# Kernel optimization log

Measured on AMD Instinct MI355X. Metric: run time of the kernel, lower is better.

The kernel has to match this reference:

```python
import jax, jax.numpy as jnp
import numpy as np

EPS = 1e-05


def setup_inputs() -> dict:
    key = jax.random.key(0)
    k1, k2 = jax.random.split(key)
    B, H, N, D = 4, 16, 4096, 128
    x = jax.random.normal(k1, (B, H, N, D), dtype=jnp.float32)
    # learned raw (non-skew) parameter; skew-symmetrized in reference
    S_raw = jax.random.normal(k2, (H, D, D), dtype=jnp.float32) * 0.05
    return {"x": x, "S_raw": S_raw}


def reference(x, S_raw):
    # x: (B, H, N, D); S_raw: (H, D, D)
    B, H, N, D = x.shape
    S = S_raw - jnp.swapaxes(S_raw, -1, -2)          # skew-symmetric (H, D, D)
    I = jnp.eye(D, dtype=x.dtype)
    A = (1.0 + EPS) * I + S                           # I + S + eps*I
    Bmat = I - S
    # rhs: (H, D, B*N) matching torch permute/reshape/transpose
    rhs = x.transpose(1, 3, 0, 2).reshape(H, D, B * N)
    y0 = jnp.linalg.solve(A, rhs)                     # batched solve over H
    y = Bmat @ y0                                     # (H, D, B*N)
    y = y.reshape(H, D, B, N).transpose(2, 0, 3, 1)   # (B, H, N, D)
    return y
```

## Files before the change

kernel.cpp:

```cpp
#include <hip/hip_runtime.h>
#include <stdint.h>

typedef __attribute__((ext_vector_type(4))) float floatx4;
typedef __attribute__((ext_vector_type(8))) short shortx8;
typedef __attribute__((ext_vector_type(2))) __bf16 bf16x2;

#define EPSF 1e-5f

#if defined(__has_builtin)
#if __has_builtin(__builtin_amdgcn_cvt_pk_bf16_f32)
#define HAVE_CVT_PK_BF16 1
#endif
#if __has_builtin(__builtin_amdgcn_rcpf)
#define HAVE_RCPF 1
#endif
#endif

__device__ __forceinline__ unsigned int pack2_bf16(float a, float b) {
#ifdef HAVE_CVT_PK_BF16
    bf16x2 r = __builtin_amdgcn_cvt_pk_bf16_f32(a, b);
    union { bf16x2 v; unsigned int u; } cv; cv.v = r; return cv.u;
#else
    unsigned int ua = __float_as_uint(a), ub = __float_as_uint(b);
    ua = (ua + 0x7fffu + ((ua >> 16) & 1u)) >> 16;
    ub = (ub + 0x7fffu + ((ub >> 16) & 1u)) & 0xffff0000u;
    return ub | ua;
#endif
}

__device__ __forceinline__ float fast_rcp(float x) {
#ifdef HAVE_RCPF
    return __builtin_amdgcn_rcpf(x);
#else
    return 1.0f / x;
#endif
}

__global__ __launch_bounds__(512) void cayley_invert(
    const float* __restrict__ S_raw, unsigned short* __restrict__ Mb)
{
    const int h  = blockIdx.x;
    const int t  = threadIdx.x;
    const int i  = t >> 2;
    const int s  = t & 3;
    const int j0 = s << 5;
    const float* Sr = S_raw + (size_t)h * 16384;

    float loc[32];
#pragma unroll
    for (int m = 0; m < 32; ++m) {
        const int j = j0 + m;
        float v = Sr[i * 128 + j] - Sr[j * 128 + i];
        if (j == i) v += 1.0f + EPSF;
        loc[m] = v;
    }

    __shared__ __align__(16) float rowbuf[2][128];
    __shared__ float dumbuf[2][128];

    if (i == 0) {
#pragma unroll
        for (int q = 0; q < 8; ++q) {
            floatx4 w;
            w[0] = loc[q*4+0]; w[1] = loc[q*4+1]; w[2] = loc[q*4+2]; w[3] = loc[q*4+3];
            if (q == 0 && s == 0) w[0] += 1.0f;
            *(floatx4*)(&rowbuf[0][j0 + q*4]) = w;
        }
    }
    if (s == 0) {
        float dv = loc[0];
        if (i == 0) dv -= 1.0f;
        dumbuf[0][i] = dv;
    }
    __syncthreads();

    for (int kb = 0; kb < 4; ++kb) {
#pragma unroll
        for (int kk = 0; kk < 32; ++kk) {
            const int cur = kk & 1;
            const int nxt = cur ^ 1;
            const int k   = (kb << 5) + kk;

            const float wk  = rowbuf[cur][k];
            const float dum = dumbuf[cur][i];
            const float akk = wk - 1.0f;
            const float de  = dum * fast_rcp(akk);

            floatx4 rv[8];
#pragma unroll
            for (int q = 0; q < 8; ++q)
                rv[q] = *(const floatx4*)(&rowbuf[cur][j0 + q*4]);

#pragma unroll
            for (int m = 0; m < 32; ++m)
                loc[m] = fmaf(-de, rv[m >> 2][m & 3], loc[m]);

            const int kn = k + 1;
            if (kn < 128) {
                const int sp   = (kk == 31) ? kb + 1 : kb;
                const int mloc = (kk == 31) ? 0 : kk + 1;
                const int qm   = mloc >> 2, em = mloc & 3;

                if (i == kn) {
#pragma unroll
                    for (int q = 0; q < 8; ++q) {
                        floatx4 w;
                        w[0] = loc[q*4+0]; w[1] = loc[q*4+1];
                        w[2] = loc[q*4+2]; w[3] = loc[q*4+3];
                        if (q == qm && s == sp) w[em] += 1.0f;
                        *(floatx4*)(&rowbuf[nxt][j0 + q*4]) = w;
                    }
                }
                if (s == sp) {
                    float dv = loc[mloc];
                    if (i == kn) dv -= 1.0f;
                    dumbuf[nxt][i] = dv;
                }
            }
            __syncthreads();
        }
    }

    unsigned short* dst = Mb + (size_t)h * 16384 + i * 128 + j0;
#pragma unroll
    for (int q = 0; q < 4; ++q) {
        union { shortx8 v; unsigned int u[4]; } cv;
#pragma unroll
        for (int p = 0; p < 4; ++p) {
            const int m = q*8 + p*2;
            const float v0 = (2.0f + EPSF) * loc[m]   - ((j0 + m   == i) ? 1.0f : 0.0f);
            const float v1 = (2.0f + EPSF) * loc[m+1] - ((j0 + m+1 == i) ? 1.0f : 0.0f);
            cv.u[p] = pack2_bf16(v0, v1);
        }
        *(shortx8*)(dst + q*8) = cv.v;
    }
}

__global__ __launch_bounds__(256, 4) void cayley_apply(
    const float* __restrict__ x, const unsigned short* __restrict__ Mb,
    float* __restrict__ y)
{
    const int bid  = blockIdx.x;
    const int bh   = bid >> 5;
    const int g    = bid & 31;
    const int h    = bh & 15;
    const int tid  = threadIdx.x;
    const int w    = tid >> 6;
    const int lane = tid & 63;
    const int l15  = lane & 15;
    const int quad = lane >> 4;

    __shared__ __align__(16) unsigned short Msh[2048 * 8];

    {
        const unsigned short* Mg = Mb + (size_t)h * 16384;
#pragma unroll
        for (int it = 0; it < 8; ++it) {
            const int c  = tid + it * 256;
            const int ct = c >> 8;
            const int ks = (c >> 6) & 3;
            const int qd = (c >> 4) & 3;
            const int r  = (ct << 4) | (c & 15);
            const int gq = (ks << 2) | qd;
            *(shortx8*)(&Msh[c * 8]) = *(const shortx8*)(Mg + r * 128 + gq * 8);
        }
    }
    __syncthreads();

    const size_t base = (size_t)bh * (4096 * 128);
    const int row0    = g * 128 + w * 32;
    const float* xw   = x + base + (size_t)(row0 + l15) * 128 + quad * 8;

#pragma unroll
    for (int t = 0; t < 2; ++t) {
        const float* xt = xw + t * (16 * 128);

        floatx4 xa[8];
#pragma unroll
        for (int ks = 0; ks < 4; ++ks) {
            xa[ks*2+0] = *(const floatx4*)(xt + ks*32);
            xa[ks*2+1] = *(const floatx4*)(xt + ks*32 + 4);
        }

        shortx8 xf[4];
#pragma unroll
        for (int ks = 0; ks < 4; ++ks) {
            const floatx4 a = xa[ks*2+0];
            const floatx4 b = xa[ks*2+1];
            union { shortx8 v; unsigned int u[4]; } cv;
            cv.u[0] = pack2_bf16(a[0], a[1]);
            cv.u[1] = pack2_bf16(a[2], a[3]);
            cv.u[2] = pack2_bf16(b[0], b[1]);
            cv.u[3] = pack2_bf16(b[2], b[3]);
            xf[ks] = cv.v;
        }

        floatx4 acc[8];
#pragma unroll
        for (int ct = 0; ct < 8; ++ct) acc[ct] = (floatx4)0.0f;

#pragma unroll
        for (int ks = 0; ks < 4; ++ks) {
#pragma unroll
            for (int ct = 0; ct < 8; ++ct) {
                const shortx8 mf = *(const shortx8*)(&Msh[((((ct << 2) | ks) << 6) | lane) * 8]);
                acc[ct] = __builtin_amdgcn_mfma_f32_16x16x32_bf16(mf, xf[ks], acc[ct], 0, 0, 0);
            }
        }

        float* yt = y + base + (size_t)(row0 + t*16 + l15) * 128 + quad * 4;
#pragma unroll
        for (int ct = 0; ct < 8; ++ct)
            __builtin_nontemporal_store(acc[ct], (floatx4*)(yt + ct*16));
    }
}

extern "C" void kernel_launch(void* const* d_in, const int* in_sizes, int n_in,
                              void* d_out, int out_size, void* d_ws, size_t ws_size,
                              hipStream_t stream) {
    const float* x     = (const float*)d_in[0];
    const float* S_raw = (const float*)d_in[1];
    float* y = (float*)d_out;
    unsigned short* Mb = (unsigned short*)d_ws;

    cayley_invert<<<16, 512, 0, stream>>>(S_raw, Mb);
    cayley_apply<<<64 * 32, 256, 0, stream>>>(x, Mb, y);
}
```

Baseline: 319.3 us.

## Eliminate two pivots per step in inversion and hoist x loads in apply

The Gauss-Jordan inversion now processes two pivot rows per iteration using a 2x2 block update, halving the number of __syncthreads barriers in the serial 128-step elimination. Each thread does more arithmetic per step and more shared buffers are maintained. In the apply kernel all x loads for both tiles are issued up front so more memory requests are in flight, and the output uses regular stores instead of nontemporal stores. The changes risk numerical differences from the blocked pivoting and higher register pressure.

```diff
diff --git a/kernel.cpp b/kernel.cpp
--- a/kernel.cpp
+++ b/kernel.cpp
@@ -55,66 +55,96 @@
         loc[m] = v;
     }
 
-    __shared__ __align__(16) float rowbuf[2][128];
-    __shared__ float dumbuf[2][128];
+    __shared__ __align__(16) float w1buf[2][128];
+    __shared__ __align__(16) float r2buf[2][128];
+    __shared__ float d1buf[2][128];
+    __shared__ float c2buf[2][128];
 
     if (i == 0) {
 #pragma unroll
         for (int q = 0; q < 8; ++q) {
             floatx4 w;
-            w[0] = loc[q*4+0]; w[1] = loc[q*4+1]; w[2] = loc[q*4+2]; w[3] = loc[q*4+3];
+            w[0]=loc[q*4+0]; w[1]=loc[q*4+1]; w[2]=loc[q*4+2]; w[3]=loc[q*4+3];
             if (q == 0 && s == 0) w[0] += 1.0f;
-            *(floatx4*)(&rowbuf[0][j0 + q*4]) = w;
+            *(floatx4*)(&w1buf[0][j0 + q*4]) = w;
+        }
+    }
+    if (i == 1) {
+#pragma unroll
+        for (int q = 0; q < 8; ++q) {
+            floatx4 w;
+            w[0]=loc[q*4+0]; w[1]=loc[q*4+1]; w[2]=loc[q*4+2]; w[3]=loc[q*4+3];
+            *(floatx4*)(&r2buf[0][j0 + q*4]) = w;
         }
     }
     if (s == 0) {
         float dv = loc[0];
         if (i == 0) dv -= 1.0f;
-        dumbuf[0][i] = dv;
+        d1buf[0][i] = dv;
+        c2buf[0][i] = loc[1];
     }
     __syncthreads();
 
     for (int kb = 0; kb < 4; ++kb) {
 #pragma unroll
-        for (int kk = 0; kk < 32; ++kk) {
+        for (int kk = 0; kk < 16; ++kk) {
             const int cur = kk & 1;
             const int nxt = cur ^ 1;
-            const int k   = (kb << 5) + kk;
-
-            const float wk  = rowbuf[cur][k];
-            const float dum = dumbuf[cur][i];
-            const float akk = wk - 1.0f;
-            const float de  = dum * fast_rcp(akk);
-
-            floatx4 rv[8];
-#pragma unroll
-            for (int q = 0; q < 8; ++q)
-                rv[q] = *(const floatx4*)(&rowbuf[cur][j0 + q*4]);
-
-#pragma unroll
-            for (int m = 0; m < 32; ++m)
-                loc[m] = fmaf(-de, rv[m >> 2][m & 3], loc[m]);
-
-            const int kn = k + 1;
+            const int k   = (kb << 5) + (kk << 1);
+
+            const float w1k  = w1buf[cur][k];
+            const float rp1  = fast_rcp(w1k - 1.0f);
+            const float e1   = d1buf[cur][i] * rp1;
+            const float qc   = d1buf[cur][k + 1] * rp1;
+            const float w1k1 = w1buf[cur][k + 1];
+            const float p2   = r2buf[cur][k + 1] - qc * w1k1;
+            const float rp2  = fast_rcp(p2);
+            const float c2p  = c2buf[cur][i] - e1 * w1k1;
+            const float e2   = (c2p - ((i == k + 1) ? 1.0f : 0.0f)) * rp2;
+
+            floatx4 w1v[8], r2v[8];
+#pragma unroll
+            for (int q = 0; q < 8; ++q) {
+                w1v[q] = *(const floatx4*)(&w1buf[cur][j0 + q*4]);
+                r2v[q] = *(const floatx4*)(&r2buf[cur][j0 + q*4]);
+            }
+#pragma unroll
+            for (int m = 0; m < 32; ++m) {
+                const float w1m = w1v[m >> 2][m & 3];
+                const float r2p = fmaf(-qc, w1m, r2v[m >> 2][m & 3]);
+                loc[m] = fmaf(-e2, r2p, fmaf(-e1, w1m, loc[m]));
+            }
+            if (s == kb) loc[(kk << 1) + 1] -= e2;
+
+            const int kn = k + 2;
             if (kn < 128) {
-                const int sp   = (kk == 31) ? kb + 1 : kb;
-                const int mloc = (kk == 31) ? 0 : kk + 1;
-                const int qm   = mloc >> 2, em = mloc & 3;
+                const int sp = (kk == 15) ? kb + 1 : kb;
+                const int m2 = (kk == 15) ? 0 : (kk << 1) + 2;
+                const int m3 = m2 + 1;
+                const int q2 = m2 >> 2, f2 = m2 & 3;
 
                 if (i == kn) {
 #pragma unroll
                     for (int q = 0; q < 8; ++q) {
                         floatx4 w;
-                        w[0] = loc[q*4+0]; w[1] = loc[q*4+1];
-                        w[2] = loc[q*4+2]; w[3] = loc[q*4+3];
-                        if (q == qm && s == sp) w[em] += 1.0f;
-                        *(floatx4*)(&rowbuf[nxt][j0 + q*4]) = w;
+                        w[0]=loc[q*4+0]; w[1]=loc[q*4+1]; w[2]=loc[q*4+2]; w[3]=loc[q*4+3];
+                        if (q == q2 && s == sp) w[f2] += 1.0f;
+                        *(floatx4*)(&w1buf[nxt][j0 + q*4]) = w;
+                    }
+                }
+                if (i == kn + 1) {
+#pragma unroll
+                    for (int q = 0; q < 8; ++q) {
+                        floatx4 w;
+                        w[0]=loc[q*4+0]; w[1]=loc[q*4+1]; w[2]=loc[q*4+2]; w[3]=loc[q*4+3];
+                        *(floatx4*)(&r2buf[nxt][j0 + q*4]) = w;
                     }
                 }
                 if (s == sp) {
-                    float dv = loc[mloc];
+                    float dv = loc[m2];
                     if (i == kn) dv -= 1.0f;
-                    dumbuf[nxt][i] = dv;
+                    d1buf[nxt][i] = dv;
+                    c2buf[nxt][i] = loc[m3];
                 }
             }
             __syncthreads();
@@ -171,22 +201,23 @@
     const int row0    = g * 128 + w * 32;
     const float* xw   = x + base + (size_t)(row0 + l15) * 128 + quad * 8;
 
+    floatx4 xa[2][8];
 #pragma unroll
     for (int t = 0; t < 2; ++t) {
-        const float* xt = xw + t * (16 * 128);
-
-        floatx4 xa[8];
 #pragma unroll
         for (int ks = 0; ks < 4; ++ks) {
-            xa[ks*2+0] = *(const floatx4*)(xt + ks*32);
-            xa[ks*2+1] = *(const floatx4*)(xt + ks*32 + 4);
-        }
-
+            xa[t][ks*2+0] = *(const floatx4*)(xw + t*2048 + ks*32);
+            xa[t][ks*2+1] = *(const floatx4*)(xw + t*2048 + ks*32 + 4);
+        }
+    }
+
+#pragma unroll
+    for (int t = 0; t < 2; ++t) {
         shortx8 xf[4];
 #pragma unroll
         for (int ks = 0; ks < 4; ++ks) {
-            const floatx4 a = xa[ks*2+0];
-            const floatx4 b = xa[ks*2+1];
+            const floatx4 a = xa[t][ks*2+0];
+            const floatx4 b = xa[t][ks*2+1];
             union { shortx8 v; unsigned int u[4]; } cv;
             cv.u[0] = pack2_bf16(a[0], a[1]);
             cv.u[1] = pack2_bf16(a[2], a[3]);
@@ -211,7 +242,7 @@
         float* yt = y + base + (size_t)(row0 + t*16 + l15) * 128 + quad * 4;
 #pragma unroll
         for (int ct = 0; ct < 8; ++ct)
-            __builtin_nontemporal_store(acc[ct], (floatx4*)(yt + ct*16));
+            *(floatx4*)(yt + ct*16) = acc[ct];
     }
 }
 
```

Measured after the change: 305.3 us. 4.4% less time.
